# Kernel tuning notes

Measured on AMD Instinct MI355X. Metric: run time of the kernel, lower is better.

Reference implementation:

```python
import jax, jax.numpy as jnp
import numpy as np

B, T, D, H = 64, 1024, 512, 512
_SCALE = 1.0 / np.sqrt(H)  # torch-style RNNCell init scale


def setup_inputs() -> dict:
    key = jax.random.key(0)
    ks = jax.random.split(key, 9)
    f32 = jnp.float32
    return {
        "x": jax.random.normal(ks[0], (B, T, D), dtype=f32),
        "Wih_f": jax.random.normal(ks[1], (H, D), dtype=f32) * _SCALE,
        "Whh_f": jax.random.normal(ks[2], (H, H), dtype=f32) * _SCALE,
        "bih_f": jax.random.normal(ks[3], (H,), dtype=f32) * _SCALE,
        "bhh_f": jax.random.normal(ks[4], (H,), dtype=f32) * _SCALE,
        "Wih_b": jax.random.normal(ks[5], (H, D), dtype=f32) * _SCALE,
        "Whh_b": jax.random.normal(ks[6], (H, H), dtype=f32) * _SCALE,
        "bih_b": jax.random.normal(ks[7], (H,), dtype=f32) * _SCALE,
        "bhh_b": jax.random.normal(ks[8], (H,), dtype=f32) * _SCALE,
    }


def _scan_direction(x_bt, Wih, Whh, bih, bhh):
    # x_bt: [B, T, D] already in processing order for this direction.
    # Precompute the input projection for all timesteps (one big GEMM),
    # leaving only the recurrent GEMM inside the scan.
    xp = jnp.einsum('btd,hd->bth', x_bt, Wih) + bih + bhh  # [B, T, H]
    h0 = jnp.zeros((x_bt.shape[0], Whh.shape[0]), dtype=x_bt.dtype)

    def step(h, xt):  # xt: [B, H]
        h_new = jnp.tanh(xt + h @ Whh.T)
        return h_new, h_new

    _, hs = jax.lax.scan(step, h0, jnp.swapaxes(xp, 0, 1))  # hs: [T, B, H]
    return jnp.swapaxes(hs, 0, 1)  # [B, T, H] in processing order


def reference(x, Wih_f, Whh_f, bih_f, bhh_f, Wih_b, Whh_b, bih_b, bhh_b):
    # Forward direction: timesteps 0..T-1.
    fh = _scan_direction(x, Wih_f, Whh_f, bih_f, bhh_f)
    # Backward direction: cell consumes x reversed in time; torch code appends
    # hiddens in processing order (i.e., index t <-> original time T-1-t).
    bh = _scan_direction(x[:, ::-1, :], Wih_b, Whh_b, bih_b, bhh_b)
    # output_last=False branch: [B, 2, T, H]
    return jnp.stack([fh, bh], axis=1)
```

## Files before the change

kernel.cpp:

```cpp
#include <hip/hip_runtime.h>
#include <hip/hip_fp16.h>
#include <cstdint>

typedef _Float16 h2 __attribute__((ext_vector_type(2)));
typedef _Float16 h8 __attribute__((ext_vector_type(8)));
typedef float    f4 __attribute__((ext_vector_type(4)));
typedef uint32_t u4 __attribute__((ext_vector_type(4)));

#define BATCH 64
#define TSTEPS 1024
#define DDIM 512
#define HDIM 512

static __device__ __forceinline__ float fdot2(uint32_t w, uint32_t h, float acc) {
  return __builtin_amdgcn_fdot2(__builtin_bit_cast(h2, w), __builtin_bit_cast(h2, h), acc, false);
}

#define BAR_LDS()                                            \
  do {                                                       \
    __builtin_amdgcn_sched_barrier(0);                       \
    asm volatile("s_waitcnt lgkmcnt(0)" ::: "memory");       \
    __builtin_amdgcn_s_barrier();                            \
    __builtin_amdgcn_sched_barrier(0);                       \
  } while (0)

__global__ void prep_kernel(const float* __restrict__ Wih_f, const float* __restrict__ Whh_f,
                            const float* __restrict__ bih_f, const float* __restrict__ bhh_f,
                            const float* __restrict__ Wih_b, const float* __restrict__ Whh_b,
                            const float* __restrict__ bih_b, const float* __restrict__ bhh_b,
                            _Float16* __restrict__ wi16, uint32_t* __restrict__ whT,
                            float* __restrict__ bsum) {
  int i = blockIdx.x * 256 + threadIdx.x;
  if (i < 2 * 512 * 512) {
    const float* s = (i < 512 * 512) ? Wih_f : Wih_b;
    wi16[i] = (_Float16)s[i & (512 * 512 - 1)];
  }
  if (i < 2 * 256 * 512) {
    int d = i >> 17; int rem = i & ((1 << 17) - 1);
    int kp = rem >> 9; int j = rem & 511;
    const float* W = d ? Whh_b : Whh_f;
    h2 p; p[0] = (_Float16)W[j * 512 + 2 * kp]; p[1] = (_Float16)W[j * 512 + 2 * kp + 1];
    whT[i] = __builtin_bit_cast(uint32_t, p);
  }
  if (i < 2 * 512) {
    int d = i >> 9, j = i & 511;
    bsum[i] = d ? (bih_b[j] + bhh_b[j]) : (bih_f[j] + bhh_f[j]);
  }
}

__global__ __launch_bounds__(256) void xp_gemm(const float* __restrict__ x,
                                               const _Float16* __restrict__ wi,
                                               const float* __restrict__ bsum,
                                               _Float16* __restrict__ xp) {
  __shared__ _Float16 As[128][40];
  __shared__ _Float16 Bs[128][40];
  const int mt = blockIdx.x, nt = blockIdx.y, dir = blockIdx.z;
  const int m0 = mt * 128, n0 = nt * 128;
  const int tid = threadIdx.x;
  const int lane = tid & 63, w = tid >> 6;
  const int wr = w >> 1, wc = w & 1;
  const int ra = tid >> 1, hf = tid & 1;

  const int mrow = m0 + ra;
  const int bb = mrow >> 10, pp = mrow & 1023;
  const int srow = dir ? ((bb << 10) + (1023 - pp)) : mrow;
  const float*    xbase = x + (size_t)srow * 512 + hf * 16;
  const _Float16* wbase = wi + (size_t)dir * 512 * 512 + (size_t)(n0 + ra) * 512 + hf * 16;

  f4 acc[4][4];
  #pragma unroll
  for (int a = 0; a < 4; ++a)
    #pragma unroll
    for (int b = 0; b < 4; ++b) acc[a][b] = (f4)0.f;

  for (int k0 = 0; k0 < 512; k0 += 32) {
    f4 x0 = *(const f4*)(xbase + k0);
    f4 x1 = *(const f4*)(xbase + k0 + 4);
    f4 x2 = *(const f4*)(xbase + k0 + 8);
    f4 x3 = *(const f4*)(xbase + k0 + 12);
    h8 b0 = *(const h8*)(wbase + k0);
    h8 b1 = *(const h8*)(wbase + k0 + 8);
    h8 a0, a1;
    #pragma unroll
    for (int u = 0; u < 4; ++u) {
      a0[u] = (_Float16)x0[u]; a0[4 + u] = (_Float16)x1[u];
      a1[u] = (_Float16)x2[u]; a1[4 + u] = (_Float16)x3[u];
    }
    __syncthreads();
    *(h8*)&As[ra][hf * 16]     = a0;
    *(h8*)&As[ra][hf * 16 + 8] = a1;
    *(h8*)&Bs[ra][hf * 16]     = b0;
    *(h8*)&Bs[ra][hf * 16 + 8] = b1;
    __syncthreads();
    h8 af[4], bf[4];
    #pragma unroll
    for (int fm = 0; fm < 4; ++fm)
      af[fm] = *(const h8*)&As[wr * 64 + fm * 16 + (lane & 15)][(lane >> 4) * 8];
    #pragma unroll
    for (int fn = 0; fn < 4; ++fn)
      bf[fn] = *(const h8*)&Bs[wc * 64 + fn * 16 + (lane & 15)][(lane >> 4) * 8];
    #pragma unroll
    for (int fm = 0; fm < 4; ++fm)
      #pragma unroll
      for (int fn = 0; fn < 4; ++fn)
        acc[fm][fn] = __builtin_amdgcn_mfma_f32_16x16x32_f16(af[fm], bf[fn], acc[fm][fn], 0, 0, 0);
  }

  float bsv[4];
  #pragma unroll
  for (int fn = 0; fn < 4; ++fn)
    bsv[fn] = bsum[dir * 512 + n0 + wc * 64 + fn * 16 + (lane & 15)];
  #pragma unroll
  for (int fm = 0; fm < 4; ++fm)
    #pragma unroll
    for (int fn = 0; fn < 4; ++fn)
      #pragma unroll
      for (int u = 0; u < 4; ++u) {
        int m = m0 + wr * 64 + fm * 16 + (lane >> 4) * 4 + u;
        int n = n0 + wc * 64 + fn * 16 + (lane & 15);
        xp[((size_t)dir << 25) + (size_t)m * 512 + n] = (_Float16)(acc[fm][fn][u] + bsv[fn]);
      }
}

__global__ __launch_bounds__(1024, 4) void rnn_rec(const _Float16* __restrict__ xp,
                                                   const uint32_t* __restrict__ whT,
                                                   float* __restrict__ out) {
  extern __shared__ char smem[];
  uint32_t* wl   = (uint32_t*)smem;
  uint32_t* hl   = (uint32_t*)(smem + 131072);
  float*    psum = (float*)(smem + 132096);

  const int bid = blockIdx.x;
  const int dir = bid & 1, b = bid >> 1;
  const int l = threadIdx.x;
  const int w = l >> 6, lv = l & 63;
  const int ke = w >> 1, jh = w & 1;
  const int jbase = jh * 256 + lv * 4;

  const uint32_t* wb = whT + dir * (256 * 512) + (ke * 32) * 512 + jbase;
  u4 wr_[24];
  #pragma unroll
  for (int p = 0; p < 24; ++p) wr_[p] = *(const u4*)(wb + p * 512);

  char* wlb = (char*)wl + (l >> 3) * 1024 + (l & 7) * 16;
  #pragma unroll
  for (int g = 0; g < 8; ++g)
    *(u4*)(wlb + g * 128) = *(const u4*)(wb + (24 + g) * 512);

  if (l < 256) hl[l] = 0;
  __syncthreads();

  const _Float16* xpp = xp + ((size_t)dir << 25) + ((size_t)b << 19);
  float* op = out + (((size_t)(b * 2 + dir)) << 19);

  for (int t = 0; t < TSTEPS; ++t) {
    float xpv = 0.f;
    if (l < 512) xpv = (float)xpp[(size_t)t * 512 + l];

    uint32_t hvl = hl[ke * 32 + (lv & 31)];
    uint32_t hs[32];
    #pragma unroll
    for (int p = 0; p < 32; ++p) hs[p] = __builtin_amdgcn_readlane(hvl, p);

    f4 acc = (f4)0.f;
    #pragma unroll
    for (int p = 0; p < 24; ++p) {
      #pragma unroll
      for (int i = 0; i < 4; ++i) acc[i] = fdot2(wr_[p][i], hs[p], acc[i]);
    }
    #pragma unroll
    for (int g = 0; g < 8; ++g) {
      u4 wv = *(const u4*)(wlb + g * 128);
      #pragma unroll
      for (int i = 0; i < 4; ++i) acc[i] = fdot2(wv[i], hs[24 + g], acc[i]);
    }
    *(f4*)&psum[ke * 512 + jbase] = acc;
    BAR_LDS();

    if (l < 512) {
      float s0 = psum[l]          + psum[512 + l];
      float s1 = psum[1024 + l]   + psum[1536 + l];
      float s2 = psum[2048 + l]   + psum[2560 + l];
      float s3 = psum[3072 + l]   + psum[3584 + l];
      float s = ((s0 + s1) + (s2 + s3)) + xpv;
      float e = __expf(2.f * s);
      float hv = 1.f - 2.f * __builtin_amdgcn_rcpf(e + 1.f);
      op[(size_t)t * 512 + l] = hv;
      ((_Float16*)hl)[l] = (_Float16)hv;
    }
    BAR_LDS();
  }
}

extern "C" void kernel_launch(void* const* d_in, const int* in_sizes, int n_in,
                              void* d_out, int out_size, void* d_ws, size_t ws_size,
                              hipStream_t stream) {
  const float* x     = (const float*)d_in[0];
  const float* Wih_f = (const float*)d_in[1];
  const float* Whh_f = (const float*)d_in[2];
  const float* bih_f = (const float*)d_in[3];
  const float* bhh_f = (const float*)d_in[4];
  const float* Wih_b = (const float*)d_in[5];
  const float* Whh_b = (const float*)d_in[6];
  const float* bih_b = (const float*)d_in[7];
  const float* bhh_b = (const float*)d_in[8];

  char* ws = (char*)d_ws;
  _Float16* xp16 = (_Float16*)ws;
  _Float16* wi16 = (_Float16*)(ws + 134217728);
  uint32_t* whT  = (uint32_t*)(ws + 135266304);
  float*    bsum = (float*)(ws + 136314880);
  float* out = (float*)d_out;

  prep_kernel<<<2048, 256, 0, stream>>>(Wih_f, Whh_f, bih_f, bhh_f,
                                        Wih_b, Whh_b, bih_b, bhh_b, wi16, whT, bsum);
  dim3 g(512, 4, 2);
  xp_gemm<<<g, 256, 0, stream>>>(x, wi16, bsum, xp16);

  const int REC_LDS = 148480;
  hipFuncSetAttribute((const void*)rnn_rec, hipFuncAttributeMaxDynamicSharedMemorySize, REC_LDS);
  rnn_rec<<<128, 1024, REC_LDS, stream>>>(xp16, whT, out);
}
```

Baseline: 1.742 ms.

## Restructure recurrent kernel to 256 threads each owning two full output columns

The recurrent kernel moves from 1024 threads splitting the K dimension (with an LDS partial-sum reduction and two barriers per step) to 256 threads, each computing two complete hidden outputs over all K. Three quarters of the Whh weights are held in registers (384 VGPRs per thread) and the rest in LDS. The hidden state is double-buffered so only one barrier is needed per timestep. This removes the cross-wave reduction and one barrier, but serializes 256 dot2 ops per thread per step on fewer waves, with high register pressure and a risk of spills.

Result: slower. 4.586 ms (+163.2%).

```diff
diff --git a/kernel.cpp b/kernel.cpp
--- a/kernel.cpp
+++ b/kernel.cpp
@@ -4,6 +4,7 @@
 
 typedef _Float16 h2 __attribute__((ext_vector_type(2)));
 typedef _Float16 h8 __attribute__((ext_vector_type(8)));
+typedef float    f2 __attribute__((ext_vector_type(2)));
 typedef float    f4 __attribute__((ext_vector_type(4)));
 typedef uint32_t u4 __attribute__((ext_vector_type(4)));
 
@@ -122,72 +123,77 @@
       }
 }
 
-__global__ __launch_bounds__(1024, 4) void rnn_rec(const _Float16* __restrict__ xp,
-                                                   const uint32_t* __restrict__ whT,
-                                                   float* __restrict__ out) {
+__global__ __launch_bounds__(256, 1) void rnn_rec(const _Float16* __restrict__ xp,
+                                                  const uint32_t* __restrict__ whT,
+                                                  float* __restrict__ out) {
   extern __shared__ char smem[];
   uint32_t* wl   = (uint32_t*)smem;
-  uint32_t* hl   = (uint32_t*)(smem + 131072);
-  float*    psum = (float*)(smem + 132096);
+  uint32_t* hbuf = (uint32_t*)(smem + 131072);
 
   const int bid = blockIdx.x;
   const int dir = bid & 1, b = bid >> 1;
   const int l = threadIdx.x;
-  const int w = l >> 6, lv = l & 63;
-  const int ke = w >> 1, jh = w & 1;
-  const int jbase = jh * 256 + lv * 4;
-
-  const uint32_t* wb = whT + dir * (256 * 512) + (ke * 32) * 512 + jbase;
-  u4 wr_[24];
-  #pragma unroll
-  for (int p = 0; p < 24; ++p) wr_[p] = *(const u4*)(wb + p * 512);
-
-  char* wlb = (char*)wl + (l >> 3) * 1024 + (l & 7) * 16;
-  #pragma unroll
-  for (int g = 0; g < 8; ++g)
-    *(u4*)(wlb + g * 128) = *(const u4*)(wb + (24 + g) * 512);
-
-  if (l < 256) hl[l] = 0;
+  const int lv = l & 63;
+
+  const uint32_t* wb = whT + dir * (256 * 512) + 2 * l;
+
+  uint32_t w0[192], w1[192];
+  #pragma unroll
+  for (int q = 0; q < 192; ++q) {
+    uint2 v = *(const uint2*)(wb + q * 512);
+    w0[q] = v.x; w1[q] = v.y;
+  }
+
+  char* wlb = (char*)wl + (l >> 3) * 4096 + (l & 7) * 16;
+  #pragma unroll
+  for (int s = 0; s < 32; ++s) {
+    uint2 a = *(const uint2*)(wb + (192 + 2 * s) * 512);
+    uint2 c = *(const uint2*)(wb + (193 + 2 * s) * 512);
+    u4 v; v[0] = a.x; v[1] = a.y; v[2] = c.x; v[3] = c.y;
+    *(u4*)(wlb + s * 128) = v;
+  }
+  hbuf[l] = 0;
   __syncthreads();
 
   const _Float16* xpp = xp + ((size_t)dir << 25) + ((size_t)b << 19);
   float* op = out + (((size_t)(b * 2 + dir)) << 19);
 
   for (int t = 0; t < TSTEPS; ++t) {
-    float xpv = 0.f;
-    if (l < 512) xpv = (float)xpp[(size_t)t * 512 + l];
-
-    uint32_t hvl = hl[ke * 32 + (lv & 31)];
-    uint32_t hs[32];
-    #pragma unroll
-    for (int p = 0; p < 32; ++p) hs[p] = __builtin_amdgcn_readlane(hvl, p);
-
-    f4 acc = (f4)0.f;
-    #pragma unroll
-    for (int p = 0; p < 24; ++p) {
-      #pragma unroll
-      for (int i = 0; i < 4; ++i) acc[i] = fdot2(wr_[p][i], hs[p], acc[i]);
+    uint32_t xv = *(const uint32_t*)((const char*)xpp + (size_t)t * 1024 + 4 * l);
+
+    const uint32_t* hp = hbuf + (t & 1) * 256;
+    u4 hv = *(const u4*)(hp + 4 * lv);
+
+    float a0 = 0.f, a1 = 0.f;
+
+    #pragma unroll
+    for (int q = 0; q < 192; ++q) {
+      uint32_t hs = __builtin_amdgcn_readlane(hv[q & 3], q >> 2);
+      a0 = fdot2(w0[q], hs, a0);
+      a1 = fdot2(w1[q], hs, a1);
     }
     #pragma unroll
-    for (int g = 0; g < 8; ++g) {
-      u4 wv = *(const u4*)(wlb + g * 128);
-      #pragma unroll
-      for (int i = 0; i < 4; ++i) acc[i] = fdot2(wv[i], hs[24 + g], acc[i]);
+    for (int s = 0; s < 32; ++s) {
+      u4 wv = *(const u4*)(wlb + s * 128);
+      const int p0 = 192 + 2 * s, p1 = 193 + 2 * s;
+      uint32_t h0 = __builtin_amdgcn_readlane(hv[p0 & 3], p0 >> 2);
+      uint32_t h1 = __builtin_amdgcn_readlane(hv[p1 & 3], p1 >> 2);
+      a0 = fdot2(wv[0], h0, a0);
+      a1 = fdot2(wv[1], h0, a1);
+      a0 = fdot2(wv[2], h1, a0);
+      a1 = fdot2(wv[3], h1, a1);
     }
-    *(f4*)&psum[ke * 512 + jbase] = acc;
-    BAR_LDS();
-
-    if (l < 512) {
-      float s0 = psum[l]          + psum[512 + l];
-      float s1 = psum[1024 + l]   + psum[1536 + l];
-      float s2 = psum[2048 + l]   + psum[2560 + l];
-      float s3 = psum[3072 + l]   + psum[3584 + l];
-      float s = ((s0 + s1) + (s2 + s3)) + xpv;
-      float e = __expf(2.f * s);
-      float hv = 1.f - 2.f * __builtin_amdgcn_rcpf(e + 1.f);
-      op[(size_t)t * 512 + l] = hv;
-      ((_Float16*)hl)[l] = (_Float16)hv;
-    }
+
+    h2 xh = __builtin_bit_cast(h2, xv);
+    float s0 = a0 + (float)xh[0];
+    float s1 = a1 + (float)xh[1];
+    float h0 = 1.f - 2.f * __builtin_amdgcn_rcpf(__expf(2.f * s0) + 1.f);
+    float h1 = 1.f - 2.f * __builtin_amdgcn_rcpf(__expf(2.f * s1) + 1.f);
+    f2 o; o[0] = h0; o[1] = h1;
+    *(f2*)(op + (size_t)t * 512 + 2 * l) = o;
+    h2 pk; pk[0] = (_Float16)h0; pk[1] = (_Float16)h1;
+    hbuf[((t + 1) & 1) * 256 + l] = __builtin_bit_cast(uint32_t, pk);
+
     BAR_LDS();
   }
 }
@@ -217,7 +223,7 @@
   dim3 g(512, 4, 2);
   xp_gemm<<<g, 256, 0, stream>>>(x, wi16, bsum, xp16);
 
-  const int REC_LDS = 148480;
-  hipFuncSetAttribute((const void*)rnn_rec, hipFuncAttributeMaxDynamicSharedMemorySize, REC_LDS);
-  rnn_rec<<<128, 1024, REC_LDS, stream>>>(xp16, whT, out);
-}
+  const int REC_LDS = 133120;
+  (void)hipFuncSetAttribute((const void*)rnn_rec, hipFuncAttributeMaxDynamicSharedMemorySize, REC_LDS);
+  rnn_rec<<<128, 256, REC_LDS, stream>>>(xp16, whT, out);
+}
```
